# Kernel tuning notes

Hardware: AMD Instinct MI355X
Metric: run time of the kernel (lower is better)

Reference implementation:

```python
import jax, jax.numpy as jnp
import numpy as np

B, S, D = 8, 2048, 768
NEG_SLOPE = 0.2  # PyG GATConv default LeakyReLU slope


def setup_inputs() -> dict:
    key = jax.random.key(0)
    ks = jax.random.split(key, 8)
    scale = 0.02
    return {
        "hidden_states": jax.random.normal(ks[0], (B, S, D), jnp.float32),
        "transformer_output": jax.random.normal(ks[1], (B, S, D), jnp.float32),
        "W_gat": jax.random.normal(ks[2], (D, D), jnp.float32) * scale,
        "a_src": jax.random.normal(ks[3], (D,), jnp.float32) * scale,
        "a_dst": jax.random.normal(ks[4], (D,), jnp.float32) * scale,
        "b_gat": jnp.zeros((D,), jnp.float32),
        "W_fus": jax.random.normal(ks[5], (2 * D, D), jnp.float32) * scale,
        "b_fus": jnp.zeros((D,), jnp.float32),
    }


def reference(hidden_states, transformer_output, W_gat, a_src, a_dst, b_gat, W_fus, b_fus):
    # GATConv (heads=1) over a complete graph (build_graph gives all i!=j edges,
    # PyG GATConv then adds self-loops) => dense softmax attention over all S nodes.
    xp = jnp.einsum("bsd,de->bse", hidden_states, W_gat)          # [B,S,D] transformed nodes
    alpha_src = jnp.einsum("bsd,d->bs", xp, a_src)                # score contrib of source j
    alpha_dst = jnp.einsum("bsd,d->bs", xp, a_dst)                # score contrib of target i
    # e[b,i,j] = LeakyReLU(alpha_dst[b,i] + alpha_src[b,j])
    e = jax.nn.leaky_relu(alpha_dst[:, :, None] + alpha_src[:, None, :], NEG_SLOPE)
    attn = jax.nn.softmax(e, axis=-1)                              # softmax over sources j per target i
    graph_out = jnp.einsum("bij,bjd->bid", attn, xp) + b_gat       # aggregate + bias
    fused = jnp.concatenate([transformer_output, graph_out], axis=-1)
    return jnp.einsum("bsf,fd->bsd", fused, W_fus) + b_fus
```

## Files before the change

kernel.cpp:

```cpp
#include <hip/hip_runtime.h>
#include <hip/hip_bf16.h>
#include <stdint.h>

#define B_   8
#define S_   2048
#define D_   768
#define BS_  16384
#define F_   1536

typedef __attribute__((ext_vector_type(8))) short short8;
typedef __attribute__((ext_vector_type(4))) float f32x4;
typedef __attribute__((ext_vector_type(4))) float float4v;
typedef __attribute__((ext_vector_type(4))) unsigned short ushort4v;

__device__ __forceinline__ unsigned short f2bf(float f) {
  union { float f; unsigned u; } v; v.f = f;
  unsigned r = v.u + 0x7FFFu + ((v.u >> 16) & 1u);
  return (unsigned short)(r >> 16);
}
__device__ __forceinline__ float bf2f(unsigned short h) {
  union { unsigned u; float f; } v; v.u = ((unsigned)h) << 16;
  return v.f;
}
__device__ __forceinline__ unsigned cvtpk_bf16(float lo, float hi) {
  unsigned r; asm("v_cvt_pk_bf16_f32 %0, %1, %2" : "=v"(r) : "v"(lo), "v"(hi)); return r;
}

#define GLOAD16(gp, lp) \
  __builtin_amdgcn_global_load_lds((const __attribute__((address_space(1))) void*)(gp), \
                                   (__attribute__((address_space(3))) void*)(lp), 16, 0, 0)

__global__ __launch_bounds__(256) void k_cast8x2(const float* __restrict__ s1,
                                                 const float* __restrict__ s2,
                                                 unsigned short* __restrict__ d1,
                                                 unsigned short* __restrict__ d2, int n) {
  int i = (blockIdx.x * 256 + threadIdx.x) * 8;
  if (i >= n) return;
  {
    float4v a = *(const float4v*)(s1 + i);
    float4v b2 = *(const float4v*)(s1 + i + 4);
    union { short8 s; unsigned u[4]; } o;
    o.u[0] = cvtpk_bf16(a[0], a[1]); o.u[1] = cvtpk_bf16(a[2], a[3]);
    o.u[2] = cvtpk_bf16(b2[0], b2[1]); o.u[3] = cvtpk_bf16(b2[2], b2[3]);
    *(short8*)(d1 + i) = o.s;
  }
  {
    float4v a = *(const float4v*)(s2 + i);
    float4v b2 = *(const float4v*)(s2 + i + 4);
    union { short8 s; unsigned u[4]; } o;
    o.u[0] = cvtpk_bf16(a[0], a[1]); o.u[1] = cvtpk_bf16(a[2], a[3]);
    o.u[2] = cvtpk_bf16(b2[0], b2[1]); o.u[3] = cvtpk_bf16(b2[2], b2[3]);
    *(short8*)(d2 + i) = o.s;
  }
}

__global__ __launch_bounds__(256) void k_transpose_cast(const float* __restrict__ src,
                                                        unsigned short* __restrict__ dst,
                                                        int R, int C) {
  __shared__ float tile[32][33];
  int bx = blockIdx.x * 32;
  int by = blockIdx.y * 32;
  int tx = threadIdx.x, ty = threadIdx.y;
#pragma unroll
  for (int k = 0; k < 32; k += 8)
    tile[ty + k][tx] = src[(size_t)(by + ty + k) * C + bx + tx];
  __syncthreads();
#pragma unroll
  for (int k = 0; k < 32; k += 8)
    dst[(size_t)(bx + ty + k) * R + by + tx] = f2bf(tile[tx][ty + k]);
}

template <int EPI>
__global__ __launch_bounds__(256, 2) void k_gemm(const unsigned short* __restrict__ A,
                                                 const unsigned short* __restrict__ A2,
                                                 const unsigned short* __restrict__ BT,
                                                 int K, int Ksplit,
                                                 float* __restrict__ outF,
                                                 const float* __restrict__ bias,
                                                 unsigned short* __restrict__ outT) {
  __shared__ unsigned short smem[32768];
  int lin = blockIdx.x;
  int nl  = (lin & 7) * 96 + (lin >> 3);
  int mBase = (nl / 6) * 128;
  int nBase = (nl % 6) * 128;
  int t = threadIdx.x;
  int w = t >> 6, l = t & 63;
  int lm = l & 15, lg = l >> 4;
  int wm = w >> 1, wn = w & 1;
  f32x4 acc[4][4] = {};
  const int KT = K >> 6;

  auto stage = [&](int kt, int half) {
    unsigned short* Ab = smem + half * 16384;
    unsigned short* Bb = Ab + 8192;
    const unsigned short* As = (kt < Ksplit) ? A : A2;
    int ka = (kt < Ksplit) ? kt : kt - Ksplit;
#pragma unroll
    for (int i = 0; i < 4; ++i) {
      int g = i * 256 + t;
      int r = g >> 3;
      int c = (g & 7) ^ (r & 7);
      GLOAD16(As + (size_t)(mBase + r) * 768 + ka + c * 8, (char*)Ab + i * 4096 + w * 1024);
      GLOAD16(BT + (size_t)(nBase + r) * K + kt + c * 8, (char*)Bb + i * 4096 + w * 1024);
    }
  };

  stage(0, 0);
  for (int kt = 0; kt < KT; ++kt) {
    int half = kt & 1;
    if (kt + 1 < KT) {
      stage((kt + 1) * 64, half ^ 1);
      asm volatile("s_waitcnt vmcnt(8)" ::: "memory");
    } else {
      asm volatile("s_waitcnt vmcnt(0)" ::: "memory");
    }
    __builtin_amdgcn_s_barrier();
    __builtin_amdgcn_sched_barrier(0);
    unsigned short* Ab = smem + half * 16384;
    unsigned short* Bb = Ab + 8192;
    __builtin_amdgcn_s_setprio(1);
#pragma unroll
    for (int ks = 0; ks < 2; ++ks) {
      short8 af[4], bfr[4];
#pragma unroll
      for (int mi = 0; mi < 4; ++mi) {
        int r = wm * 64 + mi * 16 + lm;
        int c = (ks * 4 + lg) ^ (r & 7);
        af[mi] = *(const short8*)(Ab + r * 64 + c * 8);
      }
#pragma unroll
      for (int ni = 0; ni < 4; ++ni) {
        int r = wn * 64 + ni * 16 + lm;
        int c = (ks * 4 + lg) ^ (r & 7);
        bfr[ni] = *(const short8*)(Bb + r * 64 + c * 8);
      }
#pragma unroll
      for (int mi = 0; mi < 4; ++mi)
#pragma unroll
        for (int ni = 0; ni < 4; ++ni)
          acc[mi][ni] = __builtin_amdgcn_mfma_f32_16x16x32_bf16(af[mi], bfr[ni], acc[mi][ni], 0, 0, 0);
    }
    __builtin_amdgcn_s_setprio(0);
    __builtin_amdgcn_sched_barrier(0);
    __builtin_amdgcn_s_barrier();
  }

  if (EPI == 0) {
#pragma unroll
    for (int mi = 0; mi < 4; ++mi) {
      int m = mBase + wm * 64 + mi * 16 + lg * 4;
#pragma unroll
      for (int ni = 0; ni < 4; ++ni) {
        int n = nBase + wn * 64 + ni * 16 + lm;
        float bv = bias[n];
#pragma unroll
        for (int r = 0; r < 4; ++r)
          outF[(size_t)(m + r) * 768 + n] = acc[mi][ni][r] + bv;
      }
    }
  } else {
#pragma unroll
    for (int mi = 0; mi < 4; ++mi) {
#pragma unroll
      for (int ni = 0; ni < 4; ++ni) {
        int col = wn * 64 + ni * 16 + lm;
#pragma unroll
        for (int r = 0; r < 4; ++r) {
          int row = wm * 64 + mi * 16 + lg * 4 + r;
          int phys = (((col >> 3) ^ (row & 7)) << 3) | (col & 7);
          smem[row * 128 + phys] = f2bf(acc[mi][ni][r]);
        }
      }
    }
    __syncthreads();
#pragma unroll
    for (int it = 0; it < 8; ++it) {
      int row = it * 16 + (t >> 4);
      int gg = t & 15;
      short8 v = *(const short8*)(&smem[row * 128 + ((gg ^ (row & 7)) << 3)]);
      *(short8*)(outT + (size_t)(mBase + row) * 768 + nBase + gg * 8) = v;
    }
  }
}

__global__ __launch_bounds__(256) void k_alphas(const unsigned short* __restrict__ xp,
                                                const float* __restrict__ a_src,
                                                const float* __restrict__ a_dst,
                                                float* __restrict__ as, float* __restrict__ ad) {
  int b = blockIdx.y;
  int w = threadIdx.x >> 6, lane = threadIdx.x & 63;
  float sv[12], dv[12];
#pragma unroll
  for (int q = 0; q < 3; ++q) {
    *(float4v*)(sv + q * 4) = *(const float4v*)(a_src + lane * 12 + q * 4);
    *(float4v*)(dv + q * 4) = *(const float4v*)(a_dst + lane * 12 + q * 4);
  }
  int r0 = blockIdx.x * 64 + w * 16;
  for (int rr = 0; rr < 16; ++rr) {
    int row = r0 + rr;
    const unsigned short* px = xp + ((size_t)b * S_ + row) * D_ + lane * 12;
    float accs = 0.f, accd = 0.f;
#pragma unroll
    for (int q = 0; q < 3; ++q) {
      ushort4v xv = *(const ushort4v*)(px + q * 4);
#pragma unroll
      for (int e = 0; e < 4; ++e) {
        float x = bf2f(xv[e]);
        accs = fmaf(sv[q * 4 + e], x, accs);
        accd = fmaf(dv[q * 4 + e], x, accd);
      }
    }
#pragma unroll
    for (int m = 32; m; m >>= 1) {
      accs += __shfl_xor(accs, m);
      accd += __shfl_xor(accd, m);
    }
    if (lane == 0) { as[b * S_ + row] = accs; ad[b * S_ + row] = accd; }
  }
}

__global__ __launch_bounds__(256) void k_rank(const float* __restrict__ as,
                                              float* __restrict__ ssorted, int* __restrict__ sidx,
                                              float* __restrict__ es1g, float* __restrict__ es2g,
                                              float* __restrict__ msg) {
  __shared__ float sjl[S_];
  __shared__ float red[256];
  __shared__ int rk[32][9];
  int b = blockIdx.y, t = threadIdx.x;
  float lmx = -1e30f;
#pragma unroll
  for (int q = 0; q < 2; ++q) {
    int p = (t + q * 256) * 4;
    float4v v = *(const float4v*)(as + b * S_ + p);
    *(float4v*)(sjl + p) = v;
    lmx = fmaxf(lmx, fmaxf(fmaxf(v[0], v[1]), fmaxf(v[2], v[3])));
  }
  red[t] = lmx;
  __syncthreads();
  for (int st = 128; st > 0; st >>= 1) {
    if (t < st) red[t] = fmaxf(red[t], red[t + st]);
    __syncthreads();
  }
  float Ms = red[0];
  int jl = t & 31, part = t >> 5;
  int j = blockIdx.x * 32 + jl;
  float sj = sjl[j];
  int r0 = 0, r1 = 0, r2 = 0, r3 = 0;
  int kbase = part * 256;
#pragma unroll 8
  for (int kq = 0; kq < 64; ++kq) {
    int k = kbase + kq * 4;
    float4v sk = *(const float4v*)(sjl + k);
    r0 += (sk[0] < sj) | ((sk[0] == sj) & (k < j));
    r1 += (sk[1] < sj) | ((sk[1] == sj) & (k + 1 < j));
    r2 += (sk[2] < sj) | ((sk[2] == sj) & (k + 2 < j));
    r3 += (sk[3] < sj) | ((sk[3] == sj) & (k + 3 < j));
  }
  rk[jl][part] = r0 + r1 + r2 + r3;
  __syncthreads();
  if (t < 32) {
    int rank = rk[t][0] + rk[t][1] + rk[t][2] + rk[t][3]
             + rk[t][4] + rk[t][5] + rk[t][6] + rk[t][7];
    int jj = blockIdx.x * 32 + t;
    float sv = sjl[jj];
    ssorted[b * S_ + rank] = sv;
    sidx[b * S_ + rank] = jj;
    es1g[b * S_ + rank] = __expf(sv - Ms);
    es2g[b * S_ + rank] = __expf(0.2f * (sv - Ms));
    if (blockIdx.x == 0 && t == 0) msg[b] = Ms;
  }
}

__global__ __launch_bounds__(256) void k_pscan(const float* __restrict__ es1g,
                                               const float* __restrict__ es2g,
                                               float* __restrict__ sufug,
                                               float* __restrict__ prevg) {
  __shared__ float su[256], pv[256];
  int b = blockIdx.x, t = threadIdx.x;
  float a1 = 0.f, a2 = 0.f;
#pragma unroll
  for (int r = 0; r < 8; ++r) {
    a1 += es1g[b * S_ + t * 8 + r];
    a2 += es2g[b * S_ + t * 8 + r];
  }
  su[t] = a1; pv[t] = a2;
  __syncthreads();
  for (int off = 1; off < 256; off <<= 1) {
    float vs = (t + off < 256) ? su[t + off] : 0.f;
    float vp = (t >= off) ? pv[t - off] : 0.f;
    __syncthreads();
    su[t] += vs; pv[t] += vp;
    __syncthreads();
  }
  sufug[b * 260 + t] = su[t];
  prevg[b * 260 + t] = (t > 0) ? pv[t - 1] : 0.f;
  if (t == 0) sufug[b * 260 + 256] = 0.f;
}

__global__ __launch_bounds__(192) void k_chunks(const unsigned short* __restrict__ xp,
                                                const int* __restrict__ sidx,
                                                const float* __restrict__ es1g,
                                                const float* __restrict__ es2g,
                                                float* __restrict__ SU, float* __restrict__ SV) {
  __shared__ int ridx[64];
  __shared__ float w1l[64], w2l[64];
  int b = blockIdx.y, cblk = blockIdx.x;
  int t = threadIdx.x;
  if (t < 64) {
    int r = cblk * 64 + t;
    ridx[t] = sidx[b * S_ + r];
    w1l[t] = es1g[b * S_ + r];
    w2l[t] = es2g[b * S_ + r];
  }
  __syncthreads();
  int d0 = t * 4;
  const unsigned short* xb = xp + (size_t)b * S_ * D_;
  for (int q = 0; q < 8; ++q) {
    float a1[4] = {0.f, 0.f, 0.f, 0.f}, a2[4] = {0.f, 0.f, 0.f, 0.f};
#pragma unroll
    for (int r = 0; r < 8; ++r) {
      int j = q * 8 + r;
      ushort4v xv = *(const ushort4v*)(xb + (size_t)ridx[j] * D_ + d0);
      float w1 = w1l[j], w2 = w2l[j];
#pragma unroll
      for (int e = 0; e < 4; ++e) {
        float x = bf2f(xv[e]);
        a1[e] = fmaf(w1, x, a1[e]);
        a2[e] = fmaf(w2, x, a2[e]);
      }
    }
    int c = cblk * 8 + q;
    float4v o1, o2;
    o1[0] = a1[0]; o1[1] = a1[1]; o1[2] = a1[2]; o1[3] = a1[3];
    o2[0] = a2[0]; o2[1] = a2[1]; o2[2] = a2[2]; o2[3] = a2[3];
    *(float4v*)(SU + ((size_t)b * 257 + c) * D_ + d0) = o1;
    *(float4v*)(SV + ((size_t)b * 256 + c) * D_ + d0) = o2;
  }
}

__global__ __launch_bounds__(256) void k_scan(float* __restrict__ SU, float* __restrict__ SV) {
  __shared__ float sums[8][33];
  int b = blockIdx.y;
  int dl = threadIdx.x & 31, p = threadIdx.x >> 5;
  int d = blockIdx.x * 32 + dl;
  float* u = SU + (size_t)b * 257 * D_ + d;
  float* v = SV + (size_t)b * 256 * D_ + d;
  int c0 = p * 32;
  float cu[32], cv[32];
  float su_ = 0.f, sv_ = 0.f;
#pragma unroll
  for (int q = 0; q < 32; ++q) {
    cu[q] = u[(size_t)(c0 + q) * D_];
    cv[q] = v[(size_t)(c0 + q) * D_];
    su_ += cu[q]; sv_ += cv[q];
  }
  sums[p][dl] = su_;
  __syncthreads();
  float offU = 0.f;
#pragma unroll
  for (int q = 0; q < 8; ++q) if (q > p) offU += sums[q][dl];
  __syncthreads();
  sums[p][dl] = sv_;
  __syncthreads();
  float offV = 0.f;
#pragma unroll
  for (int q = 0; q < 8; ++q) if (q < p) offV += sums[q][dl];
  float run = offU;
#pragma unroll
  for (int q = 31; q >= 0; --q) { run += cu[q]; u[(size_t)(c0 + q) * D_] = run; }
  float pr = offV;
#pragma unroll
  for (int q = 0; q < 32; ++q) { v[(size_t)(c0 + q) * D_] = pr; pr += cv[q]; }
  if (p == 0) u[(size_t)256 * D_] = 0.f;
}

__global__ __launch_bounds__(256) void k_out(const unsigned short* __restrict__ xp,
                                             const float* __restrict__ ad,
                                             const float* __restrict__ ssorted,
                                             const int* __restrict__ sidx,
                                             const float* __restrict__ es1g,
                                             const float* __restrict__ es2g,
                                             const float* __restrict__ sufug,
                                             const float* __restrict__ prevg,
                                             const float* __restrict__ msg,
                                             const float* __restrict__ SU,
                                             const float* __restrict__ SV,
                                             const float* __restrict__ b_gat,
                                             unsigned short* __restrict__ gout) {
  __shared__ float skeys[2048];
  __shared__ float G1[16], G2[16], WL[16][8];
  __shared__ int CI[16], RI[16][8];
  int bid = blockIdx.x;
  int b = bid & 7, itile = bid >> 3;
  int i0 = itile * 16;
  int t = threadIdx.x;
#pragma unroll
  for (int k2 = 0; k2 < 2; ++k2) {
    int p = (t + k2 * 256) * 4;
    *(float4v*)(skeys + p) = *(const float4v*)(ssorted + b * S_ + p);
  }
  __syncthreads();
  if (t < 16) {
    int i = i0 + t;
    float di = ad[b * S_ + i];
    float thr = -di;
    int lo = 0, hi = 2048;
#pragma unroll
    for (int st = 0; st < 11; ++st) {
      int mid = (lo + hi) >> 1;
      if (skeys[mid] <= thr) lo = mid + 1; else hi = mid;
    }
    int c = lo >> 3; if (c > 255) c = 255;
    float t1 = di + msg[b];
    float mst = fmaxf(t1, 0.2f * t1);
    float g1 = __expf(t1 - mst), g2 = __expf(0.2f * t1 - mst);
    float den = g1 * sufug[b * 260 + c + 1] + g2 * prevg[b * 260 + c];
    float wr[8]; int rid[8];
#pragma unroll
    for (int r = 0; r < 8; ++r) {
      int row = c * 8 + r;
      bool neg = (skeys[row] <= thr);
      float wv = neg ? g2 * es2g[b * S_ + row] : g1 * es1g[b * S_ + row];
      den += wv;
      wr[r] = wv;
      rid[r] = sidx[b * S_ + row];
    }
    float inv = 1.f / den;
    G1[t] = g1 * inv; G2[t] = g2 * inv; CI[t] = c;
#pragma unroll
    for (int r = 0; r < 8; ++r) { WL[t][r] = wr[r] * inv; RI[t][r] = rid[r]; }
  }
  __syncthreads();
  int d0 = t * 3;
  float bg0 = b_gat[d0], bg1 = b_gat[d0 + 1], bg2 = b_gat[d0 + 2];
  const unsigned short* xb = xp + (size_t)b * S_ * D_;
  const float* SUb = SU + (size_t)b * 257 * D_;
  const float* SVb = SV + (size_t)b * 256 * D_;
  for (int ii = 0; ii < 16; ++ii) {
    int c = CI[ii];
    float g1 = G1[ii], g2 = G2[ii];
    const float* urow = SUb + (size_t)(c + 1) * D_ + d0;
    const float* vrow = SVb + (size_t)c * D_ + d0;
    float o0 = fmaf(g1, urow[0], g2 * vrow[0]);
    float o1 = fmaf(g1, urow[1], g2 * vrow[1]);
    float o2 = fmaf(g1, urow[2], g2 * vrow[2]);
#pragma unroll
    for (int r = 0; r < 8; ++r) {
      float wv = WL[ii][r];
      const unsigned short* xr = xb + (size_t)RI[ii][r] * D_ + d0;
      o0 = fmaf(wv, bf2f(xr[0]), o0);
      o1 = fmaf(wv, bf2f(xr[1]), o1);
      o2 = fmaf(wv, bf2f(xr[2]), o2);
    }
    unsigned short* go = gout + ((size_t)b * S_ + i0 + ii) * D_ + d0;
    go[0] = f2bf(o0 + bg0); go[1] = f2bf(o1 + bg1); go[2] = f2bf(o2 + bg2);
  }
}

extern "C" void kernel_launch(void* const* d_in, const int* in_sizes, int n_in,
                              void* d_out, int out_size, void* d_ws, size_t ws_size,
                              hipStream_t stream) {
  const float* hs   = (const float*)d_in[0];
  const float* to   = (const float*)d_in[1];
  const float* Wg   = (const float*)d_in[2];
  const float* asrc = (const float*)d_in[3];
  const float* adst = (const float*)d_in[4];
  const float* bg   = (const float*)d_in[5];
  const float* Wf   = (const float*)d_in[6];
  const float* bfu  = (const float*)d_in[7];
  float* out = (float*)d_out;

  char* ws = (char*)d_ws;
  size_t off = 0;
  auto alloc = [&](size_t bytes) {
    char* p = ws + off;
    off += (bytes + 255) & ~(size_t)255;
    return p;
  };
  unsigned short* hs_bf = (unsigned short*)alloc((size_t)BS_ * D_ * 2);
  unsigned short* to_bf = (unsigned short*)alloc((size_t)BS_ * D_ * 2);
  unsigned short* xp    = (unsigned short*)alloc((size_t)BS_ * D_ * 2);
  unsigned short* WgT   = (unsigned short*)alloc((size_t)D_ * D_ * 2);
  unsigned short* WfT   = (unsigned short*)alloc((size_t)D_ * F_ * 2);
  float* as   = (float*)alloc((size_t)BS_ * 4);
  float* ad   = (float*)alloc((size_t)BS_ * 4);
  float* ssorted = (float*)alloc((size_t)BS_ * 4);
  int*   sidx    = (int*)alloc((size_t)BS_ * 4);
  float* es1g = (float*)alloc((size_t)BS_ * 4);
  float* es2g = (float*)alloc((size_t)BS_ * 4);
  float* sufug = (float*)alloc((size_t)B_ * 260 * 4);
  float* prevg = (float*)alloc((size_t)B_ * 260 * 4);
  float* msg   = (float*)alloc(256);
  float* SU = (float*)alloc((size_t)B_ * 257 * D_ * 4);
  float* SV = (float*)alloc((size_t)B_ * 256 * D_ * 4);
  unsigned short* gout = hs_bf;

  int n = BS_ * D_;
  k_cast8x2<<<n / 2048, 256, 0, stream>>>(hs, to, hs_bf, to_bf, n);
  k_transpose_cast<<<dim3(D_ / 32, D_ / 32), dim3(32, 8), 0, stream>>>(Wg, WgT, D_, D_);
  k_transpose_cast<<<dim3(D_ / 32, F_ / 32), dim3(32, 8), 0, stream>>>(Wf, WfT, F_, D_);
  k_gemm<1><<<768, 256, 0, stream>>>(hs_bf, hs_bf, WgT, D_, D_, nullptr, nullptr, xp);
  k_alphas<<<dim3(32, B_), 256, 0, stream>>>(xp, asrc, adst, as, ad);
  k_rank<<<dim3(64, B_), 256, 0, stream>>>(as, ssorted, sidx, es1g, es2g, msg);
  k_pscan<<<B_, 256, 0, stream>>>(es1g, es2g, sufug, prevg);
  k_chunks<<<dim3(32, B_), 192, 0, stream>>>(xp, sidx, es1g, es2g, SU, SV);
  k_scan<<<dim3(24, B_), 256, 0, stream>>>(SU, SV);
  k_out<<<1024, 256, 0, stream>>>(xp, ad, ssorted, sidx, es1g, es2g, sufug, prevg, msg,
                                  SU, SV, bg, gout);
  k_gemm<0><<<768, 256, 0, stream>>>(to_bf, gout, WfT, F_, D_, out, bfu, nullptr);
}
```

Baseline: 179.8 us.

## Fuse alpha dot products into GAT GEMM epilogue and move transformer cast into k_out

Result: no change. 176.4 us (-1.9%).

```diff
diff --git a/kernel.cpp b/kernel.cpp
--- a/kernel.cpp
+++ b/kernel.cpp
@@ -30,28 +30,16 @@
   __builtin_amdgcn_global_load_lds((const __attribute__((address_space(1))) void*)(gp), \
                                    (__attribute__((address_space(3))) void*)(lp), 16, 0, 0)
 
-__global__ __launch_bounds__(256) void k_cast8x2(const float* __restrict__ s1,
-                                                 const float* __restrict__ s2,
-                                                 unsigned short* __restrict__ d1,
-                                                 unsigned short* __restrict__ d2, int n) {
+__global__ __launch_bounds__(256) void k_cast8(const float* __restrict__ s1,
+                                               unsigned short* __restrict__ d1, int n) {
   int i = (blockIdx.x * 256 + threadIdx.x) * 8;
   if (i >= n) return;
-  {
-    float4v a = *(const float4v*)(s1 + i);
-    float4v b2 = *(const float4v*)(s1 + i + 4);
-    union { short8 s; unsigned u[4]; } o;
-    o.u[0] = cvtpk_bf16(a[0], a[1]); o.u[1] = cvtpk_bf16(a[2], a[3]);
-    o.u[2] = cvtpk_bf16(b2[0], b2[1]); o.u[3] = cvtpk_bf16(b2[2], b2[3]);
-    *(short8*)(d1 + i) = o.s;
-  }
-  {
-    float4v a = *(const float4v*)(s2 + i);
-    float4v b2 = *(const float4v*)(s2 + i + 4);
-    union { short8 s; unsigned u[4]; } o;
-    o.u[0] = cvtpk_bf16(a[0], a[1]); o.u[1] = cvtpk_bf16(a[2], a[3]);
-    o.u[2] = cvtpk_bf16(b2[0], b2[1]); o.u[3] = cvtpk_bf16(b2[2], b2[3]);
-    *(short8*)(d2 + i) = o.s;
-  }
+  float4v a = *(const float4v*)(s1 + i);
+  float4v b2 = *(const float4v*)(s1 + i + 4);
+  union { short8 s; unsigned u[4]; } o;
+  o.u[0] = cvtpk_bf16(a[0], a[1]); o.u[1] = cvtpk_bf16(a[2], a[3]);
+  o.u[2] = cvtpk_bf16(b2[0], b2[1]); o.u[3] = cvtpk_bf16(b2[2], b2[3]);
+  *(short8*)(d1 + i) = o.s;
 }
 
 __global__ __launch_bounds__(256) void k_transpose_cast(const float* __restrict__ src,
@@ -77,7 +65,11 @@
                                                  int K, int Ksplit,
                                                  float* __restrict__ outF,
                                                  const float* __restrict__ bias,
-                                                 unsigned short* __restrict__ outT) {
+                                                 unsigned short* __restrict__ outT,
+                                                 const float* __restrict__ aS,
+                                                 const float* __restrict__ aD,
+                                                 float* __restrict__ asO,
+                                                 float* __restrict__ adO) {
   __shared__ unsigned short smem[32768];
   int lin = blockIdx.x;
   int nl  = (lin & 7) * 96 + (lin >> 3);
@@ -172,6 +164,11 @@
         }
       }
     }
+    float* aLds = (float*)(smem + 16384);
+    if (t < 128) {
+      aLds[t] = aS[nBase + t];
+      aLds[128 + t] = aD[nBase + t];
+    }
     __syncthreads();
 #pragma unroll
     for (int it = 0; it < 8; ++it) {
@@ -180,42 +177,27 @@
       short8 v = *(const short8*)(&smem[row * 128 + ((gg ^ (row & 7)) << 3)]);
       *(short8*)(outT + (size_t)(mBase + row) * 768 + nBase + gg * 8) = v;
     }
-  }
-}
-
-__global__ __launch_bounds__(256) void k_alphas(const unsigned short* __restrict__ xp,
-                                                const float* __restrict__ a_src,
-                                                const float* __restrict__ a_dst,
-                                                float* __restrict__ as, float* __restrict__ ad) {
-  int b = blockIdx.y;
-  int w = threadIdx.x >> 6, lane = threadIdx.x & 63;
-  float sv[12], dv[12];
-#pragma unroll
-  for (int q = 0; q < 3; ++q) {
-    *(float4v*)(sv + q * 4) = *(const float4v*)(a_src + lane * 12 + q * 4);
-    *(float4v*)(dv + q * 4) = *(const float4v*)(a_dst + lane * 12 + q * 4);
-  }
-  int r0 = blockIdx.x * 64 + w * 16;
-  for (int rr = 0; rr < 16; ++rr) {
-    int row = r0 + rr;
-    const unsigned short* px = xp + ((size_t)b * S_ + row) * D_ + lane * 12;
-    float accs = 0.f, accd = 0.f;
-#pragma unroll
-    for (int q = 0; q < 3; ++q) {
-      ushort4v xv = *(const ushort4v*)(px + q * 4);
-#pragma unroll
-      for (int e = 0; e < 4; ++e) {
-        float x = bf2f(xv[e]);
-        accs = fmaf(sv[q * 4 + e], x, accs);
-        accd = fmaf(dv[q * 4 + e], x, accd);
-      }
-    }
-#pragma unroll
-    for (int m = 32; m; m >>= 1) {
-      accs += __shfl_xor(accs, m);
-      accd += __shfl_xor(accd, m);
-    }
-    if (lane == 0) { as[b * S_ + row] = accs; ad[b * S_ + row] = accd; }
+    {
+      int row = t >> 1, halfc = t & 1;
+      float accs = 0.f, accd = 0.f;
+#pragma unroll
+      for (int gg = 0; gg < 8; ++gg) {
+        int cq = halfc * 8 + gg;
+        short8 v = *(const short8*)(&smem[row * 128 + ((cq ^ (row & 7)) << 3)]);
+#pragma unroll
+        for (int e = 0; e < 8; ++e) {
+          float x = bf2f((unsigned short)v[e]);
+          accs = fmaf(aLds[cq * 8 + e], x, accs);
+          accd = fmaf(aLds[128 + cq * 8 + e], x, accd);
+        }
+      }
+      accs += __shfl_xor(accs, 1);
+      accd += __shfl_xor(accd, 1);
+      if (halfc == 0) {
+        atomicAdd(asO + mBase + row, accs);
+        atomicAdd(adO + mBase + row, accd);
+      }
+    }
   }
 }
 
@@ -386,6 +368,8 @@
                                              const float* __restrict__ SU,
                                              const float* __restrict__ SV,
                                              const float* __restrict__ b_gat,
+                                             const float* __restrict__ to,
+                                             unsigned short* __restrict__ to_bf,
                                              unsigned short* __restrict__ gout) {
   __shared__ float skeys[2048];
   __shared__ float G1[16], G2[16], WL[16][8];
@@ -444,6 +428,8 @@
     float o0 = fmaf(g1, urow[0], g2 * vrow[0]);
     float o1 = fmaf(g1, urow[1], g2 * vrow[1]);
     float o2 = fmaf(g1, urow[2], g2 * vrow[2]);
+    size_t roff = ((size_t)(b * S_ + i0 + ii)) * D_ + d0;
+    float t0v = to[roff], t1v = to[roff + 1], t2v = to[roff + 2];
 #pragma unroll
     for (int r = 0; r < 8; ++r) {
       float wv = WL[ii][r];
@@ -452,7 +438,9 @@
       o1 = fmaf(wv, bf2f(xr[1]), o1);
       o2 = fmaf(wv, bf2f(xr[2]), o2);
     }
-    unsigned short* go = gout + ((size_t)b * S_ + i0 + ii) * D_ + d0;
+    unsigned short* tw = to_bf + roff;
+    tw[0] = f2bf(t0v); tw[1] = f2bf(t1v); tw[2] = f2bf(t2v);
+    unsigned short* go = gout + roff;
     go[0] = f2bf(o0 + bg0); go[1] = f2bf(o1 + bg1); go[2] = f2bf(o2 + bg2);
   }
 }
@@ -496,16 +484,19 @@
   unsigned short* gout = hs_bf;
 
   int n = BS_ * D_;
-  k_cast8x2<<<n / 2048, 256, 0, stream>>>(hs, to, hs_bf, to_bf, n);
+  hipMemsetAsync(as, 0, (size_t)BS_ * 4, stream);
+  hipMemsetAsync(ad, 0, (size_t)BS_ * 4, stream);
+  k_cast8<<<n / 2048, 256, 0, stream>>>(hs, hs_bf, n);
   k_transpose_cast<<<dim3(D_ / 32, D_ / 32), dim3(32, 8), 0, stream>>>(Wg, WgT, D_, D_);
   k_transpose_cast<<<dim3(D_ / 32, F_ / 32), dim3(32, 8), 0, stream>>>(Wf, WfT, F_, D_);
-  k_gemm<1><<<768, 256, 0, stream>>>(hs_bf, hs_bf, WgT, D_, D_, nullptr, nullptr, xp);
-  k_alphas<<<dim3(32, B_), 256, 0, stream>>>(xp, asrc, adst, as, ad);
+  k_gemm<1><<<768, 256, 0, stream>>>(hs_bf, hs_bf, WgT, D_, D_, nullptr, nullptr, xp,
+                                     asrc, adst, as, ad);
   k_rank<<<dim3(64, B_), 256, 0, stream>>>(as, ssorted, sidx, es1g, es2g, msg);
   k_pscan<<<B_, 256, 0, stream>>>(es1g, es2g, sufug, prevg);
   k_chunks<<<dim3(32, B_), 192, 0, stream>>>(xp, sidx, es1g, es2g, SU, SV);
   k_scan<<<dim3(24, B_), 256, 0, stream>>>(SU, SV);
   k_out<<<1024, 256, 0, stream>>>(xp, ad, ssorted, sidx, es1g, es2g, sufug, prevg, msg,
-                                  SU, SV, bg, gout);
-  k_gemm<0><<<768, 256, 0, stream>>>(to_bf, gout, WfT, F_, D_, out, bfu, nullptr);
-}
+                                  SU, SV, bg, to, to_bf, gout);
+  k_gemm<0><<<768, 256, 0, stream>>>(to_bf, gout, WfT, F_, D_, out, bfu, nullptr,
+                                     nullptr, nullptr, nullptr, nullptr);
+}
```
